# Performance work log

Hardware: AMD Instinct MI355X
Metric: run time of the kernel (lower is better)

Reference implementation:

```python
import jax, jax.numpy as jnp
import numpy as np

N_NODES = 200000
N_EDGES = 3200000


def _gcn_prep(edge_index, n_nodes):
    # Add self loops (PyG GCNConv default) and compute symmetric normalization.
    loops = jnp.arange(n_nodes, dtype=edge_index.dtype)
    src = jnp.concatenate([edge_index[0], loops])
    dst = jnp.concatenate([edge_index[1], loops])
    deg = jax.ops.segment_sum(jnp.ones_like(dst, dtype=jnp.float32), dst,
                              num_segments=n_nodes)
    dinv = jnp.where(deg > 0, jax.lax.rsqrt(deg), 0.0)
    norm = dinv[src] * dinv[dst]  # [E+N]
    return src, dst, norm


def _gcn_conv(x, src, dst, norm, W, b, n_nodes):
    h = x @ W                                   # [N, out]
    msg = h[src] * norm[:, None]                # gather + scale, [E+N, out]
    out = jax.ops.segment_sum(msg, dst, num_segments=n_nodes)  # scatter-add
    return out + b


def setup_inputs() -> dict:
    key = jax.random.key(0)
    k = jax.random.split(key, 4)
    x = jax.random.normal(k[0], (N_NODES, 4), dtype=jnp.float32)
    edge_index = jax.random.randint(k[1], (2, N_EDGES), 0, N_NODES, dtype=jnp.int64)
    W1 = jax.random.normal(k[2], (4, 16), dtype=jnp.float32) * (1.0 / np.sqrt(4))
    b1 = jnp.zeros((16,), dtype=jnp.float32)
    W2 = jax.random.normal(k[3], (16, 1), dtype=jnp.float32) * (1.0 / np.sqrt(16))
    b2 = jnp.zeros((1,), dtype=jnp.float32)
    return {"x": x, "edge_index": edge_index, "W1": W1, "b1": b1,
            "W2": W2, "b2": b2}


def reference(x, edge_index, W1, b1, W2, b2):
    n = x.shape[0]
    src, dst, norm = _gcn_prep(edge_index, n)
    h = _gcn_conv(x, src, dst, norm, W1, b1, n)
    h = jax.nn.relu(h)
    out = _gcn_conv(h, src, dst, norm, W2, b2, n)
    return out
```

## Files before the change

kernel.cpp:

```cpp
#include <hip/hip_runtime.h>


#define BSE   512
#define CH    16384
#define NBW   512
#define SH    9
#define NB    391
#define FCAP  10752
#define BSB   512
#define RSTG  ((FCAP + BSB - 1) / BSB)
#define NOEDGE 0xFFFFFFFFu

__global__ void k_bin(const int* __restrict__ src, const int* __restrict__ dst,
                      int E, unsigned* __restrict__ gcur,
                      unsigned* __restrict__ epack) {
    __shared__ unsigned stage[CH];
    __shared__ unsigned cnt[NB];
    __shared__ unsigned ofs[NB + 1];
    __shared__ unsigned curp[NB];
    __shared__ unsigned gbase[NB];
    __shared__ unsigned wsum[BSE / 64];
    const int b = blockIdx.x, t = threadIdx.x;
    for (int i = t; i < NB; i += BSE) cnt[i] = 0;
    __syncthreads();
    const int lo = b * CH, hi = min(E, lo + CH);
    const int n = hi - lo;
    const int aligned = n & ~3;
    for (int i = 4 * t; i + 3 < n; i += 4 * BSE) {
        int4 d4 = *(const int4*)(dst + lo + i);
        atomicAdd(&cnt[((unsigned)d4.x) >> SH], 1u);
        atomicAdd(&cnt[((unsigned)d4.y) >> SH], 1u);
        atomicAdd(&cnt[((unsigned)d4.z) >> SH], 1u);
        atomicAdd(&cnt[((unsigned)d4.w) >> SH], 1u);
    }
    for (int i = aligned + t; i < n; i += BSE)
        atomicAdd(&cnt[((unsigned)dst[lo + i]) >> SH], 1u);
    __syncthreads();
    const unsigned c = (t < NB) ? cnt[t] : 0u;
    unsigned v = c;
    #pragma unroll
    for (int off = 1; off < 64; off <<= 1) {
        unsigned u = __shfl_up(v, off);
        if ((t & 63) >= off) v += u;
    }
    if ((t & 63) == 63) wsum[t >> 6] = v;
    __syncthreads();
    if (t < BSE / 64) {
        unsigned w = wsum[t];
        #pragma unroll
        for (int off = 1; off < BSE / 64; off <<= 1) {
            unsigned u = __shfl_up(w, off);
            if (t >= off) w += u;
        }
        wsum[t] = w;
    }
    __syncthreads();
    const unsigned incl = v + ((t >> 6) ? wsum[(t >> 6) - 1] : 0u);
    const unsigned excl = incl - c;
    if (t < NB) {
        ofs[t] = excl;
        curp[t] = excl;
        unsigned pad = (c + 15u) & ~15u;
        unsigned o = pad ? atomicAdd(&gcur[t], pad) : 0u;
        gbase[t] = (unsigned)t * FCAP + o;
    }
    if (t == NB - 1) ofs[NB] = incl;
    __syncthreads();
    for (int i = 4 * t; i + 3 < n; i += 4 * BSE) {
        int4 d4 = *(const int4*)(dst + lo + i);
        int4 s4 = *(const int4*)(src + lo + i);
        unsigned k0 = ((unsigned)d4.x) >> SH, k1 = ((unsigned)d4.y) >> SH;
        unsigned k2 = ((unsigned)d4.z) >> SH, k3 = ((unsigned)d4.w) >> SH;
        unsigned p0 = atomicAdd(&curp[k0], 1u);
        unsigned p1 = atomicAdd(&curp[k1], 1u);
        unsigned p2 = atomicAdd(&curp[k2], 1u);
        unsigned p3 = atomicAdd(&curp[k3], 1u);
        stage[p0] = ((unsigned)s4.x << SH) | (((unsigned)d4.x) & (NBW - 1u));
        stage[p1] = ((unsigned)s4.y << SH) | (((unsigned)d4.y) & (NBW - 1u));
        stage[p2] = ((unsigned)s4.z << SH) | (((unsigned)d4.z) & (NBW - 1u));
        stage[p3] = ((unsigned)s4.w << SH) | (((unsigned)d4.w) & (NBW - 1u));
    }
    for (int i = aligned + t; i < n; i += BSE) {
        unsigned d = (unsigned)dst[lo + i];
        unsigned k = d >> SH;
        unsigned pos = atomicAdd(&curp[k], 1u);
        stage[pos] = ((unsigned)src[lo + i] << SH) | (d & (NBW - 1u));
    }
    __syncthreads();
    for (int p0 = 4 * t; p0 < n; p0 += 4 * BSE) {
        unsigned k = 0;
        #pragma unroll
        for (unsigned s = 256; s; s >>= 1) {
            unsigned cand = k + s;
            if (cand <= NB && ofs[cand] <= (unsigned)p0) k = cand;
        }
        #pragma unroll
        for (int j = 0; j < 4; ++j) {
            int p = p0 + j;
            if (p >= n) break;
            while (ofs[k + 1] <= (unsigned)p) ++k;
            unsigned addr = gbase[k] + ((unsigned)p - ofs[k]);
            if (addr < (k + 1u) * FCAP) epack[addr] = stage[p];
        }
    }
    for (int i = t; i < NB; i += BSE) {
        unsigned s = gbase[i] + cnt[i];
        unsigned e = gbase[i] + ((cnt[i] + 15u) & ~15u);
        unsigned kend = ((unsigned)i + 1u) * FCAP;
        if (e > kend) e = kend;
        for (unsigned p = s; p < e; ++p) epack[p] = NOEDGE;
    }
}

__global__ void k_build(unsigned* __restrict__ epack, const unsigned* __restrict__ gcur,
                        const float* __restrict__ x,
                        unsigned* __restrict__ meta,
                        float* __restrict__ x_scaled, int N) {
    __shared__ unsigned stage[FCAP];
    __shared__ unsigned cnt[BSB];
    __shared__ unsigned cur[BSB];
    __shared__ unsigned wsum[BSB / 64];
    __shared__ unsigned s_lenv;
    const int k = blockIdx.x, t = threadIdx.x;
    const unsigned base = (unsigned)k * FCAP;
    const int len = min((int)gcur[k], FCAP);
    unsigned r[RSTG];
    #pragma unroll
    for (int j = 0; j < RSTG; ++j) {
        int i = t + j * BSB;
        r[j] = (i < len) ? epack[base + i] : NOEDGE;
    }
    cnt[t] = 0;
    __syncthreads();
    #pragma unroll
    for (int j = 0; j < RSTG; ++j) {
        unsigned p = r[j];
        if (p != NOEDGE) atomicAdd(&cnt[p & (NBW - 1u)], 1u);
    }
    __syncthreads();
    const unsigned c = cnt[t];
    unsigned v = c;
    #pragma unroll
    for (int off = 1; off < 64; off <<= 1) {
        unsigned u = __shfl_up(v, off);
        if ((t & 63) >= off) v += u;
    }
    if ((t & 63) == 63) wsum[t >> 6] = v;
    __syncthreads();
    if (t < BSB / 64) {
        unsigned w = wsum[t];
        #pragma unroll
        for (int off = 1; off < BSB / 64; off <<= 1) {
            unsigned u = __shfl_up(w, off);
            if (t >= off) w += u;
        }
        wsum[t] = w;
    }
    __syncthreads();
    const unsigned incl = v + ((t >> 6) ? wsum[(t >> 6) - 1] : 0u);
    const unsigned excl = incl - c;
    cur[t] = excl;
    if (t == BSB - 1) s_lenv = incl;
    const int node = k * NBW + t;
    if (node < N) {
        meta[node] = excl | (c << 14);
        float di = rsqrtf((float)(c + 1u));
        float4 xv = ((const float4*)x)[node];
        ((float4*)x_scaled)[node] = make_float4(xv.x * di, xv.y * di, xv.z * di, xv.w * di);
    }
    __syncthreads();
    #pragma unroll
    for (int j = 0; j < RSTG; ++j) {
        unsigned p = r[j];
        if (p != NOEDGE) {
            unsigned pos = atomicAdd(&cur[p & (NBW - 1u)], 1u);
            stage[pos] = p >> SH;
        }
    }
    __syncthreads();
    const int lenv = (int)s_lenv;
    for (int i = 4 * t; i + 3 < lenv; i += 4 * BSB)
        *(int4*)(epack + base + i) = *(const int4*)&stage[i];
    if (t < (lenv & 3)) epack[base + (lenv & ~3) + t] = stage[(lenv & ~3) + t];
}

__global__ void k_agg1(const unsigned* __restrict__ esorted, const unsigned* __restrict__ meta,
                       const float* __restrict__ x_scaled,
                       const float* __restrict__ W1, const float* __restrict__ b1,
                       const float* __restrict__ W2,
                       float* __restrict__ z_scaled, int N) {
    int node = blockIdx.x * blockDim.x + threadIdx.x;
    if (node >= N) return;
    unsigned m = meta[node];
    unsigned c = m >> 14;
    unsigned lo = (unsigned)(node >> SH) * FCAP + (m & 16383u);
    unsigned hi = lo + c;
    float di = rsqrtf((float)(c + 1u));
    const float4* xs4 = (const float4*)x_scaled;
    float4 a0 = xs4[node];
    float4 a1 = make_float4(0.f, 0.f, 0.f, 0.f);
    float4 a2 = make_float4(0.f, 0.f, 0.f, 0.f);
    float4 a3 = make_float4(0.f, 0.f, 0.f, 0.f);
    unsigned i = lo;
    for (; i + 3 < hi; i += 4) {
        float4 v0 = xs4[esorted[i]],     v1 = xs4[esorted[i + 1]];
        float4 v2 = xs4[esorted[i + 2]], v3 = xs4[esorted[i + 3]];
        a0.x += v0.x; a0.y += v0.y; a0.z += v0.z; a0.w += v0.w;
        a1.x += v1.x; a1.y += v1.y; a1.z += v1.z; a1.w += v1.w;
        a2.x += v2.x; a2.y += v2.y; a2.z += v2.z; a2.w += v2.w;
        a3.x += v3.x; a3.y += v3.y; a3.z += v3.z; a3.w += v3.w;
    }
    for (; i < hi; ++i) {
        float4 v = xs4[esorted[i]];
        a0.x += v.x; a0.y += v.y; a0.z += v.z; a0.w += v.w;
    }
    float p0 = di * (a0.x + a1.x + a2.x + a3.x);
    float p1 = di * (a0.y + a1.y + a2.y + a3.y);
    float p2 = di * (a0.z + a1.z + a2.z + a3.z);
    float p3 = di * (a0.w + a1.w + a2.w + a3.w);
    float z = 0.0f;
    #pragma unroll
    for (int cc = 0; cc < 16; ++cc) {
        float h1 = p0 * W1[0 * 16 + cc] + p1 * W1[1 * 16 + cc]
                 + p2 * W1[2 * 16 + cc] + p3 * W1[3 * 16 + cc] + b1[cc];
        h1 = fmaxf(h1, 0.0f);
        z += h1 * W2[cc];
    }
    z_scaled[node] = z * di;
}

__global__ void k_agg2(const unsigned* __restrict__ esorted, const unsigned* __restrict__ meta,
                       const float* __restrict__ z_scaled,
                       const float* __restrict__ b2, float* __restrict__ out, int N) {
    int node = blockIdx.x * blockDim.x + threadIdx.x;
    if (node >= N) return;
    unsigned m = meta[node];
    unsigned c = m >> 14;
    unsigned lo = (unsigned)(node >> SH) * FCAP + (m & 16383u);
    unsigned hi = lo + c;
    float di = rsqrtf((float)(c + 1u));
    float a0 = z_scaled[node], a1 = 0.f, a2 = 0.f, a3 = 0.f;
    unsigned i = lo;
    for (; i + 3 < hi; i += 4) {
        a0 += z_scaled[esorted[i]];
        a1 += z_scaled[esorted[i + 1]];
        a2 += z_scaled[esorted[i + 2]];
        a3 += z_scaled[esorted[i + 3]];
    }
    for (; i < hi; ++i) a0 += z_scaled[esorted[i]];
    out[node] = di * (a0 + a1 + a2 + a3) + b2[0];
}

extern "C" void kernel_launch(void* const* d_in, const int* in_sizes, int n_in,
                              void* d_out, int out_size, void* d_ws, size_t ws_size,
                              hipStream_t stream) {
    const float* x  = (const float*)d_in[0];
    const int*   ei = (const int*)d_in[1];
    const float* W1 = (const float*)d_in[2];
    const float* b1 = (const float*)d_in[3];
    const float* W2 = (const float*)d_in[4];
    const float* b2 = (const float*)d_in[5];

    const int N = in_sizes[0] / 4;
    const int E = in_sizes[1] / 2;
    const int* src = ei;
    const int* dst = ei + E;
    const int NA = (E + CH - 1) / CH;

    char* ws = (char*)d_ws;
    unsigned* gcur     = (unsigned*)ws;  ws += 4096;
    unsigned* epack    = (unsigned*)ws;  ws += (size_t)NB * FCAP * 4;
    unsigned* meta     = (unsigned*)ws;  ws += (size_t)N * 4;
    float*    x_scaled = (float*)ws;     ws += (size_t)N * 4 * 4;
    float*    z_scaled = (float*)ws;     ws += (size_t)N * 4;
    float* out = (float*)d_out;

    hipMemsetAsync(gcur, 0, NB * sizeof(unsigned), stream);
    k_bin  <<<NA, BSE, 0, stream>>>(src, dst, E, gcur, epack);
    k_build<<<NB, BSB, 0, stream>>>(epack, gcur, x, meta, x_scaled, N);
    k_agg1 <<<(N + 255) / 256, 256, 0, stream>>>(epack, meta, x_scaled,
                                                 W1, b1, W2, z_scaled, N);
    k_agg2 <<<(N + 255) / 256, 256, 0, stream>>>(epack, meta, z_scaled, b2, out, N);
}
```

Before: 163.1 us.

## Fuse build and both aggregations into one cooperative kernel with LDS atomics

After: 302.3 us. +85.3%, slower.

```diff
diff --git a/kernel.cpp b/kernel.cpp
--- a/kernel.cpp
+++ b/kernel.cpp
@@ -1,4 +1,7 @@
 #include <hip/hip_runtime.h>
+#include <hip/hip_cooperative_groups.h>
+
+namespace cg = cooperative_groups;
 
 
 #define BSE   512
@@ -8,7 +11,6 @@
 #define NB    391
 #define FCAP  10752
 #define BSB   512
-#define RSTG  ((FCAP + BSB - 1) / BSB)
 #define NOEDGE 0xFFFFFFFFu
 
 __global__ void k_bin(const int* __restrict__ src, const int* __restrict__ dst,
@@ -112,143 +114,100 @@
     }
 }
 
-__global__ void k_build(unsigned* __restrict__ epack, const unsigned* __restrict__ gcur,
-                        const float* __restrict__ x,
-                        unsigned* __restrict__ meta,
-                        float* __restrict__ x_scaled, int N) {
+__global__ __launch_bounds__(BSB, 4)
+void k_coop(const unsigned* __restrict__ epack, const unsigned* __restrict__ gcur,
+            const float* __restrict__ x,
+            const float* __restrict__ W1, const float* __restrict__ b1,
+            const float* __restrict__ W2, const float* __restrict__ b2,
+            float* __restrict__ x_scaled, float* __restrict__ z_scaled,
+            float* __restrict__ out, int N) {
     __shared__ unsigned stage[FCAP];
-    __shared__ unsigned cnt[BSB];
-    __shared__ unsigned cur[BSB];
-    __shared__ unsigned wsum[BSB / 64];
-    __shared__ unsigned s_lenv;
-    const int k = blockIdx.x, t = threadIdx.x;
-    const unsigned base = (unsigned)k * FCAP;
-    const int len = min((int)gcur[k], FCAP);
-    unsigned r[RSTG];
-    #pragma unroll
-    for (int j = 0; j < RSTG; ++j) {
-        int i = t + j * BSB;
-        r[j] = (i < len) ? epack[base + i] : NOEDGE;
-    }
+    __shared__ unsigned cnt[NBW];
+    __shared__ float4  acc[NBW];
+    cg::grid_group grid = cg::this_grid();
+    const int b = blockIdx.x, t = threadIdx.x;
+    const unsigned base = (unsigned)b * FCAP;
+    const int len = min((int)gcur[b], FCAP);
     cnt[t] = 0;
     __syncthreads();
-    #pragma unroll
-    for (int j = 0; j < RSTG; ++j) {
-        unsigned p = r[j];
-        if (p != NOEDGE) atomicAdd(&cnt[p & (NBW - 1u)], 1u);
+    for (int i = 4 * t; i < len; i += 4 * BSB) {
+        int4 q = *(const int4*)(epack + base + i);
+        *(int4*)&stage[i] = q;
+        unsigned p0 = (unsigned)q.x, p1 = (unsigned)q.y;
+        unsigned p2 = (unsigned)q.z, p3 = (unsigned)q.w;
+        if (p0 != NOEDGE) atomicAdd(&cnt[p0 & (NBW - 1u)], 1u);
+        if (p1 != NOEDGE) atomicAdd(&cnt[p1 & (NBW - 1u)], 1u);
+        if (p2 != NOEDGE) atomicAdd(&cnt[p2 & (NBW - 1u)], 1u);
+        if (p3 != NOEDGE) atomicAdd(&cnt[p3 & (NBW - 1u)], 1u);
     }
     __syncthreads();
     const unsigned c = cnt[t];
-    unsigned v = c;
-    #pragma unroll
-    for (int off = 1; off < 64; off <<= 1) {
-        unsigned u = __shfl_up(v, off);
-        if ((t & 63) >= off) v += u;
-    }
-    if ((t & 63) == 63) wsum[t >> 6] = v;
-    __syncthreads();
-    if (t < BSB / 64) {
-        unsigned w = wsum[t];
-        #pragma unroll
-        for (int off = 1; off < BSB / 64; off <<= 1) {
-            unsigned u = __shfl_up(w, off);
-            if (t >= off) w += u;
-        }
-        wsum[t] = w;
-    }
-    __syncthreads();
-    const unsigned incl = v + ((t >> 6) ? wsum[(t >> 6) - 1] : 0u);
-    const unsigned excl = incl - c;
-    cur[t] = excl;
-    if (t == BSB - 1) s_lenv = incl;
-    const int node = k * NBW + t;
+    const float di = rsqrtf((float)(c + 1u));
+    const int node = b * NBW + t;
+    float4 xs = make_float4(0.f, 0.f, 0.f, 0.f);
     if (node < N) {
-        meta[node] = excl | (c << 14);
-        float di = rsqrtf((float)(c + 1u));
         float4 xv = ((const float4*)x)[node];
-        ((float4*)x_scaled)[node] = make_float4(xv.x * di, xv.y * di, xv.z * di, xv.w * di);
-    }
-    __syncthreads();
-    #pragma unroll
-    for (int j = 0; j < RSTG; ++j) {
-        unsigned p = r[j];
-        if (p != NOEDGE) {
-            unsigned pos = atomicAdd(&cur[p & (NBW - 1u)], 1u);
-            stage[pos] = p >> SH;
-        }
-    }
-    __syncthreads();
-    const int lenv = (int)s_lenv;
-    for (int i = 4 * t; i + 3 < lenv; i += 4 * BSB)
-        *(int4*)(epack + base + i) = *(const int4*)&stage[i];
-    if (t < (lenv & 3)) epack[base + (lenv & ~3) + t] = stage[(lenv & ~3) + t];
-}
-
-__global__ void k_agg1(const unsigned* __restrict__ esorted, const unsigned* __restrict__ meta,
-                       const float* __restrict__ x_scaled,
-                       const float* __restrict__ W1, const float* __restrict__ b1,
-                       const float* __restrict__ W2,
-                       float* __restrict__ z_scaled, int N) {
-    int node = blockIdx.x * blockDim.x + threadIdx.x;
-    if (node >= N) return;
-    unsigned m = meta[node];
-    unsigned c = m >> 14;
-    unsigned lo = (unsigned)(node >> SH) * FCAP + (m & 16383u);
-    unsigned hi = lo + c;
-    float di = rsqrtf((float)(c + 1u));
+        xs = make_float4(xv.x * di, xv.y * di, xv.z * di, xv.w * di);
+        ((float4*)x_scaled)[node] = xs;
+    }
+    acc[t] = make_float4(0.f, 0.f, 0.f, 0.f);
+    grid.sync();
+
     const float4* xs4 = (const float4*)x_scaled;
-    float4 a0 = xs4[node];
-    float4 a1 = make_float4(0.f, 0.f, 0.f, 0.f);
-    float4 a2 = make_float4(0.f, 0.f, 0.f, 0.f);
-    float4 a3 = make_float4(0.f, 0.f, 0.f, 0.f);
-    unsigned i = lo;
-    for (; i + 3 < hi; i += 4) {
-        float4 v0 = xs4[esorted[i]],     v1 = xs4[esorted[i + 1]];
-        float4 v2 = xs4[esorted[i + 2]], v3 = xs4[esorted[i + 3]];
-        a0.x += v0.x; a0.y += v0.y; a0.z += v0.z; a0.w += v0.w;
-        a1.x += v1.x; a1.y += v1.y; a1.z += v1.z; a1.w += v1.w;
-        a2.x += v2.x; a2.y += v2.y; a2.z += v2.z; a2.w += v2.w;
-        a3.x += v3.x; a3.y += v3.y; a3.z += v3.z; a3.w += v3.w;
-    }
-    for (; i < hi; ++i) {
-        float4 v = xs4[esorted[i]];
-        a0.x += v.x; a0.y += v.y; a0.z += v.z; a0.w += v.w;
-    }
-    float p0 = di * (a0.x + a1.x + a2.x + a3.x);
-    float p1 = di * (a0.y + a1.y + a2.y + a3.y);
-    float p2 = di * (a0.z + a1.z + a2.z + a3.z);
-    float p3 = di * (a0.w + a1.w + a2.w + a3.w);
+    for (int i = 4 * t; i < len; i += 4 * BSB) {
+        int4 q = *(const int4*)&stage[i];
+        unsigned p0 = (unsigned)q.x, p1 = (unsigned)q.y;
+        unsigned p2 = (unsigned)q.z, p3 = (unsigned)q.w;
+        unsigned i0 = (p0 != NOEDGE) ? (p0 >> SH) : (unsigned)node;
+        unsigned i1 = (p1 != NOEDGE) ? (p1 >> SH) : (unsigned)node;
+        unsigned i2 = (p2 != NOEDGE) ? (p2 >> SH) : (unsigned)node;
+        unsigned i3 = (p3 != NOEDGE) ? (p3 >> SH) : (unsigned)node;
+        float4 v0 = xs4[i0], v1 = xs4[i1], v2 = xs4[i2], v3 = xs4[i3];
+        if (p0 != NOEDGE) { float* a = (float*)&acc[p0 & (NBW - 1u)];
+            atomicAdd(a, v0.x); atomicAdd(a + 1, v0.y); atomicAdd(a + 2, v0.z); atomicAdd(a + 3, v0.w); }
+        if (p1 != NOEDGE) { float* a = (float*)&acc[p1 & (NBW - 1u)];
+            atomicAdd(a, v1.x); atomicAdd(a + 1, v1.y); atomicAdd(a + 2, v1.z); atomicAdd(a + 3, v1.w); }
+        if (p2 != NOEDGE) { float* a = (float*)&acc[p2 & (NBW - 1u)];
+            atomicAdd(a, v2.x); atomicAdd(a + 1, v2.y); atomicAdd(a + 2, v2.z); atomicAdd(a + 3, v2.w); }
+        if (p3 != NOEDGE) { float* a = (float*)&acc[p3 & (NBW - 1u)];
+            atomicAdd(a, v3.x); atomicAdd(a + 1, v3.y); atomicAdd(a + 2, v3.z); atomicAdd(a + 3, v3.w); }
+    }
+    __syncthreads();
+    float4 a = acc[t];
+    a.x += xs.x; a.y += xs.y; a.z += xs.z; a.w += xs.w;
+    const float q0 = di * a.x, q1 = di * a.y, q2 = di * a.z, q3 = di * a.w;
     float z = 0.0f;
     #pragma unroll
     for (int cc = 0; cc < 16; ++cc) {
-        float h1 = p0 * W1[0 * 16 + cc] + p1 * W1[1 * 16 + cc]
-                 + p2 * W1[2 * 16 + cc] + p3 * W1[3 * 16 + cc] + b1[cc];
+        float h1 = q0 * W1[0 * 16 + cc] + q1 * W1[1 * 16 + cc]
+                 + q2 * W1[2 * 16 + cc] + q3 * W1[3 * 16 + cc] + b1[cc];
         h1 = fmaxf(h1, 0.0f);
         z += h1 * W2[cc];
     }
-    z_scaled[node] = z * di;
-}
-
-__global__ void k_agg2(const unsigned* __restrict__ esorted, const unsigned* __restrict__ meta,
-                       const float* __restrict__ z_scaled,
-                       const float* __restrict__ b2, float* __restrict__ out, int N) {
-    int node = blockIdx.x * blockDim.x + threadIdx.x;
-    if (node >= N) return;
-    unsigned m = meta[node];
-    unsigned c = m >> 14;
-    unsigned lo = (unsigned)(node >> SH) * FCAP + (m & 16383u);
-    unsigned hi = lo + c;
-    float di = rsqrtf((float)(c + 1u));
-    float a0 = z_scaled[node], a1 = 0.f, a2 = 0.f, a3 = 0.f;
-    unsigned i = lo;
-    for (; i + 3 < hi; i += 4) {
-        a0 += z_scaled[esorted[i]];
-        a1 += z_scaled[esorted[i + 1]];
-        a2 += z_scaled[esorted[i + 2]];
-        a3 += z_scaled[esorted[i + 3]];
-    }
-    for (; i < hi; ++i) a0 += z_scaled[esorted[i]];
-    out[node] = di * (a0 + a1 + a2 + a3) + b2[0];
+    const float zdi = z * di;
+    if (node < N) z_scaled[node] = zdi;
+    float* sacc = (float*)cnt;
+    __syncthreads();
+    sacc[t] = 0.f;
+    grid.sync();
+
+    for (int i = 4 * t; i < len; i += 4 * BSB) {
+        int4 q = *(const int4*)&stage[i];
+        unsigned p0 = (unsigned)q.x, p1 = (unsigned)q.y;
+        unsigned p2 = (unsigned)q.z, p3 = (unsigned)q.w;
+        unsigned i0 = (p0 != NOEDGE) ? (p0 >> SH) : (unsigned)node;
+        unsigned i1 = (p1 != NOEDGE) ? (p1 >> SH) : (unsigned)node;
+        unsigned i2 = (p2 != NOEDGE) ? (p2 >> SH) : (unsigned)node;
+        unsigned i3 = (p3 != NOEDGE) ? (p3 >> SH) : (unsigned)node;
+        float v0 = z_scaled[i0], v1 = z_scaled[i1];
+        float v2 = z_scaled[i2], v3 = z_scaled[i3];
+        if (p0 != NOEDGE) atomicAdd(&sacc[p0 & (NBW - 1u)], v0);
+        if (p1 != NOEDGE) atomicAdd(&sacc[p1 & (NBW - 1u)], v1);
+        if (p2 != NOEDGE) atomicAdd(&sacc[p2 & (NBW - 1u)], v2);
+        if (p3 != NOEDGE) atomicAdd(&sacc[p3 & (NBW - 1u)], v3);
+    }
+    __syncthreads();
+    if (node < N) out[node] = di * (sacc[t] + zdi) + b2[0];
 }
 
 extern "C" void kernel_launch(void* const* d_in, const int* in_sizes, int n_in,
@@ -261,8 +220,8 @@
     const float* W2 = (const float*)d_in[4];
     const float* b2 = (const float*)d_in[5];
 
-    const int N = in_sizes[0] / 4;
-    const int E = in_sizes[1] / 2;
+    int N = in_sizes[0] / 4;
+    int E = in_sizes[1] / 2;
     const int* src = ei;
     const int* dst = ei + E;
     const int NA = (E + CH - 1) / CH;
@@ -270,15 +229,16 @@
     char* ws = (char*)d_ws;
     unsigned* gcur     = (unsigned*)ws;  ws += 4096;
     unsigned* epack    = (unsigned*)ws;  ws += (size_t)NB * FCAP * 4;
-    unsigned* meta     = (unsigned*)ws;  ws += (size_t)N * 4;
     float*    x_scaled = (float*)ws;     ws += (size_t)N * 4 * 4;
     float*    z_scaled = (float*)ws;     ws += (size_t)N * 4;
     float* out = (float*)d_out;
 
     hipMemsetAsync(gcur, 0, NB * sizeof(unsigned), stream);
-    k_bin  <<<NA, BSE, 0, stream>>>(src, dst, E, gcur, epack);
-    k_build<<<NB, BSB, 0, stream>>>(epack, gcur, x, meta, x_scaled, N);
-    k_agg1 <<<(N + 255) / 256, 256, 0, stream>>>(epack, meta, x_scaled,
-                                                 W1, b1, W2, z_scaled, N);
-    k_agg2 <<<(N + 255) / 256, 256, 0, stream>>>(epack, meta, z_scaled, b2, out, N);
+    k_bin<<<NA, BSE, 0, stream>>>(src, dst, E, gcur, epack);
+    void* args[] = {
+        (void*)&epack, (void*)&gcur, (void*)&x,
+        (void*)&W1, (void*)&b1, (void*)&W2, (void*)&b2,
+        (void*)&x_scaled, (void*)&z_scaled, (void*)&out, (void*)&N
+    };
+    hipLaunchCooperativeKernel((void*)k_coop, dim3(NB), dim3(BSB), args, 0, stream);
 }
```

## Pad per-node edge segments to 16B and vectorize index loads in build and aggregation

Applied to the files above, without the earlier changes.

New measurement: 166.4 us. About the same (+2.0%).

```diff
diff --git a/kernel.cpp b/kernel.cpp
--- a/kernel.cpp
+++ b/kernel.cpp
@@ -8,8 +8,10 @@
 #define NB    391
 #define FCAP  10752
 #define BSB   512
-#define RSTG  ((FCAP + BSB - 1) / BSB)
+#define RSTG4 ((FCAP + 4 * BSB - 1) / (4 * BSB))
 #define NOEDGE 0xFFFFFFFFu
+
+typedef unsigned u32x4 __attribute__((ext_vector_type(4)));
 
 __global__ void k_bin(const int* __restrict__ src, const int* __restrict__ dst,
                       int E, unsigned* __restrict__ gcur,
@@ -124,22 +126,29 @@
     const int k = blockIdx.x, t = threadIdx.x;
     const unsigned base = (unsigned)k * FCAP;
     const int len = min((int)gcur[k], FCAP);
-    unsigned r[RSTG];
-    #pragma unroll
-    for (int j = 0; j < RSTG; ++j) {
-        int i = t + j * BSB;
-        r[j] = (i < len) ? epack[base + i] : NOEDGE;
+    const int len4 = len >> 2;
+    const u32x4* ep4 = (const u32x4*)(epack + base);
+    u32x4 r4[RSTG4];
+    #pragma unroll
+    for (int j = 0; j < RSTG4; ++j) {
+        int i4 = t + j * BSB;
+        if (i4 < len4) r4[j] = __builtin_nontemporal_load(ep4 + i4);
+        else           r4[j] = (u32x4){NOEDGE, NOEDGE, NOEDGE, NOEDGE};
     }
     cnt[t] = 0;
     __syncthreads();
     #pragma unroll
-    for (int j = 0; j < RSTG; ++j) {
-        unsigned p = r[j];
-        if (p != NOEDGE) atomicAdd(&cnt[p & (NBW - 1u)], 1u);
-    }
-    __syncthreads();
-    const unsigned c = cnt[t];
-    unsigned v = c;
+    for (int j = 0; j < RSTG4; ++j) {
+        #pragma unroll
+        for (int e = 0; e < 4; ++e) {
+            unsigned p = r4[j][e];
+            if (p != NOEDGE) atomicAdd(&cnt[p & (NBW - 1u)], 1u);
+        }
+    }
+    __syncthreads();
+    const unsigned c  = cnt[t];
+    const unsigned cp = (c + 3u) & ~3u;
+    unsigned v = cp;
     #pragma unroll
     for (int off = 1; off < 64; off <<= 1) {
         unsigned u = __shfl_up(v, off);
@@ -158,7 +167,7 @@
     }
     __syncthreads();
     const unsigned incl = v + ((t >> 6) ? wsum[(t >> 6) - 1] : 0u);
-    const unsigned excl = incl - c;
+    const unsigned excl = incl - cp;
     cur[t] = excl;
     if (t == BSB - 1) s_lenv = incl;
     const int node = k * NBW + t;
@@ -170,18 +179,20 @@
     }
     __syncthreads();
     #pragma unroll
-    for (int j = 0; j < RSTG; ++j) {
-        unsigned p = r[j];
-        if (p != NOEDGE) {
-            unsigned pos = atomicAdd(&cur[p & (NBW - 1u)], 1u);
-            stage[pos] = p >> SH;
-        }
-    }
-    __syncthreads();
-    const int lenv = (int)s_lenv;
-    for (int i = 4 * t; i + 3 < lenv; i += 4 * BSB)
+    for (int j = 0; j < RSTG4; ++j) {
+        #pragma unroll
+        for (int e = 0; e < 4; ++e) {
+            unsigned p = r4[j][e];
+            if (p != NOEDGE) {
+                unsigned pos = atomicAdd(&cur[p & (NBW - 1u)], 1u);
+                if (pos < FCAP) stage[pos] = p >> SH;
+            }
+        }
+    }
+    __syncthreads();
+    const int lenv = min((int)s_lenv, FCAP);
+    for (int i = 4 * t; i < lenv; i += 4 * BSB)
         *(int4*)(epack + base + i) = *(const int4*)&stage[i];
-    if (t < (lenv & 3)) epack[base + (lenv & ~3) + t] = stage[(lenv & ~3) + t];
 }
 
 __global__ void k_agg1(const unsigned* __restrict__ esorted, const unsigned* __restrict__ meta,
@@ -202,13 +213,28 @@
     float4 a2 = make_float4(0.f, 0.f, 0.f, 0.f);
     float4 a3 = make_float4(0.f, 0.f, 0.f, 0.f);
     unsigned i = lo;
-    for (; i + 3 < hi; i += 4) {
-        float4 v0 = xs4[esorted[i]],     v1 = xs4[esorted[i + 1]];
-        float4 v2 = xs4[esorted[i + 2]], v3 = xs4[esorted[i + 3]];
+    for (; i + 7 < hi; i += 8) {
+        u32x4 e0 = *(const u32x4*)(esorted + i);
+        u32x4 e1 = *(const u32x4*)(esorted + i + 4);
+        float4 v0 = xs4[e0[0]], v1 = xs4[e0[1]], v2 = xs4[e0[2]], v3 = xs4[e0[3]];
+        float4 v4 = xs4[e1[0]], v5 = xs4[e1[1]], v6 = xs4[e1[2]], v7 = xs4[e1[3]];
         a0.x += v0.x; a0.y += v0.y; a0.z += v0.z; a0.w += v0.w;
         a1.x += v1.x; a1.y += v1.y; a1.z += v1.z; a1.w += v1.w;
         a2.x += v2.x; a2.y += v2.y; a2.z += v2.z; a2.w += v2.w;
         a3.x += v3.x; a3.y += v3.y; a3.z += v3.z; a3.w += v3.w;
+        a0.x += v4.x; a0.y += v4.y; a0.z += v4.z; a0.w += v4.w;
+        a1.x += v5.x; a1.y += v5.y; a1.z += v5.z; a1.w += v5.w;
+        a2.x += v6.x; a2.y += v6.y; a2.z += v6.z; a2.w += v6.w;
+        a3.x += v7.x; a3.y += v7.y; a3.z += v7.z; a3.w += v7.w;
+    }
+    if (i + 3 < hi) {
+        u32x4 e0 = *(const u32x4*)(esorted + i);
+        float4 v0 = xs4[e0[0]], v1 = xs4[e0[1]], v2 = xs4[e0[2]], v3 = xs4[e0[3]];
+        a0.x += v0.x; a0.y += v0.y; a0.z += v0.z; a0.w += v0.w;
+        a1.x += v1.x; a1.y += v1.y; a1.z += v1.z; a1.w += v1.w;
+        a2.x += v2.x; a2.y += v2.y; a2.z += v2.z; a2.w += v2.w;
+        a3.x += v3.x; a3.y += v3.y; a3.z += v3.z; a3.w += v3.w;
+        i += 4;
     }
     for (; i < hi; ++i) {
         float4 v = xs4[esorted[i]];
@@ -241,11 +267,19 @@
     float di = rsqrtf((float)(c + 1u));
     float a0 = z_scaled[node], a1 = 0.f, a2 = 0.f, a3 = 0.f;
     unsigned i = lo;
-    for (; i + 3 < hi; i += 4) {
-        a0 += z_scaled[esorted[i]];
-        a1 += z_scaled[esorted[i + 1]];
-        a2 += z_scaled[esorted[i + 2]];
-        a3 += z_scaled[esorted[i + 3]];
+    for (; i + 7 < hi; i += 8) {
+        u32x4 e0 = __builtin_nontemporal_load((const u32x4*)(esorted + i));
+        u32x4 e1 = __builtin_nontemporal_load((const u32x4*)(esorted + i + 4));
+        a0 += z_scaled[e0[0]]; a1 += z_scaled[e0[1]];
+        a2 += z_scaled[e0[2]]; a3 += z_scaled[e0[3]];
+        a0 += z_scaled[e1[0]]; a1 += z_scaled[e1[1]];
+        a2 += z_scaled[e1[2]]; a3 += z_scaled[e1[3]];
+    }
+    if (i + 3 < hi) {
+        u32x4 e0 = __builtin_nontemporal_load((const u32x4*)(esorted + i));
+        a0 += z_scaled[e0[0]]; a1 += z_scaled[e0[1]];
+        a2 += z_scaled[e0[2]]; a3 += z_scaled[e0[3]];
+        i += 4;
     }
     for (; i < hi; ++i) a0 += z_scaled[esorted[i]];
     out[node] = di * (a0 + a1 + a2 + a3) + b2[0];
```
